# Kernel optimization log

Hardware: AMD Instinct MI355X
Metric: run time of the kernel (lower is better)

Reference implementation:

```python
import jax, jax.numpy as jnp
import numpy as np

B, T, D_IN = 32, 128, 32
H1, H, PEN = 1024, 2048, 1024  # linear1 out, GRU hidden, penultimate
C, P = 64, 4                   # cultivars, phenos


def setup_inputs() -> dict:
    key = jax.random.key(0)
    ks = jax.random.split(key, 22)
    s = 0.02
    inp = {}
    inp['x'] = jax.random.normal(ks[0], (B, T, D_IN), dtype=jnp.float32)
    inp['cultivar_label'] = jax.random.randint(ks[1], (B, 1), 0, C)
    inp['W1'] = jax.random.normal(ks[2], (H1, D_IN), dtype=jnp.float32) * s
    inp['b1'] = jnp.zeros((H1,), jnp.float32)
    inp['W2'] = jax.random.normal(ks[3], (H, H1), dtype=jnp.float32) * s
    inp['b2'] = jnp.zeros((H,), jnp.float32)
    # GRU weights, PyTorch layout: gates stacked (r,z,n) along dim 0
    inp['W_ih'] = jax.random.normal(ks[4], (3 * H, H), dtype=jnp.float32) * s
    inp['b_ih'] = jnp.zeros((3 * H,), jnp.float32)
    inp['W_hh'] = jax.random.normal(ks[5], (3 * H, H), dtype=jnp.float32) * s
    inp['b_hh'] = jnp.zeros((3 * H,), jnp.float32)
    inp['W3'] = jax.random.normal(ks[6], (PEN, H), dtype=jnp.float32) * s
    inp['b3'] = jnp.zeros((PEN,), jnp.float32)
    # per-cultivar expert heads (each a Linear(PEN, 1)) packed as tables
    inp['W4'] = jax.random.normal(ks[7], (C, PEN), dtype=jnp.float32) * s
    inp['b4'] = jnp.zeros((C,), jnp.float32)
    inp['W5'] = jax.random.normal(ks[8], (C, PEN), dtype=jnp.float32) * s
    inp['b5'] = jnp.zeros((C,), jnp.float32)
    inp['W6'] = jax.random.normal(ks[9], (C, PEN), dtype=jnp.float32) * s
    inp['b6'] = jnp.zeros((C,), jnp.float32)
    inp['Wp'] = jax.random.normal(ks[10], (P, C, PEN), dtype=jnp.float32) * s
    inp['bp'] = jnp.zeros((P, C), jnp.float32)
    return inp


def _gru(x_seq, W_ih, b_ih, W_hh, b_hh):
    # x_seq: [B,T,H]; PyTorch GRU gate order (r, z, n)
    Bd, Hd = x_seq.shape[0], W_hh.shape[1]
    xp = jnp.einsum('bth,gh->btg', x_seq, W_ih) + b_ih  # [B,T,3H]

    def step(h, xp_t):
        hp = h @ W_hh.T + b_hh
        xr, xz, xn = jnp.split(xp_t, 3, axis=-1)
        hr, hz, hn = jnp.split(hp, 3, axis=-1)
        r = jax.nn.sigmoid(xr + hr)
        z = jax.nn.sigmoid(xz + hz)
        n = jnp.tanh(xn + r * hn)
        h_new = (1.0 - z) * n + z * h
        return h_new, h_new

    h0 = jnp.zeros((Bd, Hd), x_seq.dtype)
    _, hs = jax.lax.scan(step, h0, jnp.swapaxes(xp, 0, 1))  # [T,B,H]
    return jnp.swapaxes(hs, 0, 1)  # [B,T,H]


def reference(x, cultivar_label, W1, b1, W2, b2, W_ih, b_ih, W_hh, b_hh,
              W3, b3, W4, b4, W5, b5, W6, b6, Wp, bp):
    out = jax.nn.relu(jnp.einsum('btd,hd->bth', x, W1) + b1)
    out = jax.nn.relu(jnp.einsum('bth,gh->btg', out, W2) + b2)
    out = _gru(out, W_ih, b_ih, W_hh, b_hh)
    out_s = jax.nn.relu(jnp.einsum('bth,ph->btp', out, W3) + b3)  # [B,T,PEN]
    labels = cultivar_label[:, 0]

    def head(W, b):  # gather expert row per sample -> [B,T,1]
        return (jnp.einsum('btd,bd->bt', out_s, W[labels]) + b[labels][:, None])[..., None]

    out_lt_10 = head(W4, b4)
    out_lt_50 = head(W5, b5)
    out_lt_90 = head(W6, b6)
    # pheno heads: Wp[:, labels] -> [P,B,PEN]
    out_ph = jax.nn.sigmoid(
        jnp.einsum('btd,pbd->pbt', out_s, Wp[:, labels]) + bp[:, labels][:, :, None]
    )[..., None]  # [P,B,T,1]
    return (out_lt_10, out_lt_50, out_lt_90, out_ph, 0)
```

## Files before the change

kernel.cpp:

```cpp
#include <hip/hip_runtime.h>
#include <hip/hip_bf16.h>
#include <math.h>


typedef __bf16 bf16_t;
typedef __bf16 bf16x4 __attribute__((ext_vector_type(4)));
typedef __bf16 bf16x8 __attribute__((ext_vector_type(8)));
typedef float  f32x4  __attribute__((ext_vector_type(4)));

static __device__ __forceinline__ void zero4(f32x4& v) {
  v[0] = 0.0f; v[1] = 0.0f; v[2] = 0.0f; v[3] = 0.0f;
}

template <typename T>
static __device__ __forceinline__ bf16x8 load8_as_bf16(const T* p);
template <>
__device__ __forceinline__ bf16x8 load8_as_bf16<bf16_t>(const bf16_t* p) {
  return *(const bf16x8*)p;
}
template <>
__device__ __forceinline__ bf16x8 load8_as_bf16<float>(const float* p) {
  bf16x8 v;
#pragma unroll
  for (int u = 0; u < 8; ++u) v[u] = (bf16_t)p[u];
  return v;
}

template <typename TA, typename TB>
__global__ __launch_bounds__(256) void gemm_bt(
    const TA* __restrict__ A, const TB* __restrict__ Bm,
    const float* __restrict__ bias, bf16_t* __restrict__ C,
    int M, int N, int K, int relu)
{
  __shared__ __align__(16) bf16_t As[128 * 32];
  __shared__ __align__(16) bf16_t Bs[128 * 32];

  const int tid  = threadIdx.x;
  const int lane = tid & 63;
  const int wave = tid >> 6;
  const int q    = lane >> 4;
  const int l15  = lane & 15;
  const int wr   = wave >> 1;
  const int wc   = wave & 1;
  const int m0   = blockIdx.y * 128;
  const int n0   = blockIdx.x * 128;

  f32x4 acc[4][4];
#pragma unroll
  for (int i = 0; i < 4; ++i)
#pragma unroll
    for (int j = 0; j < 4; ++j) zero4(acc[i][j]);

  const int se = wave * 512 + lane * 8;

  const int kt_count = K >> 5;
  for (int kt = 0; kt < kt_count; ++kt) {
    const int k0 = kt << 5;

    bf16x8 av[2], bv[2];
#pragma unroll
    for (int c = 0; c < 2; ++c) {
      const int e   = c * 2048 + se;
      const int row = e >> 5;
      const int col = e & 31;
      av[c] = load8_as_bf16<TA>(&A [(size_t)(m0 + row) * K + k0 + col]);
      bv[c] = load8_as_bf16<TB>(&Bm[(size_t)(n0 + row) * K + k0 + col]);
    }

    __syncthreads();
#pragma unroll
    for (int c = 0; c < 2; ++c) {
      *(bf16x8*)&As[c * 2048 + se] = av[c];
      *(bf16x8*)&Bs[c * 2048 + se] = bv[c];
    }
    __syncthreads();

    bf16x8 af[4], bfv[4];
#pragma unroll
    for (int i = 0; i < 4; ++i)
      af[i] = *(const bf16x8*)&As[(wr * 64 + i * 16 + l15) * 32 + q * 8];
#pragma unroll
    for (int j = 0; j < 4; ++j)
      bfv[j] = *(const bf16x8*)&Bs[(wc * 64 + j * 16 + l15) * 32 + q * 8];

#pragma unroll
    for (int i = 0; i < 4; ++i)
#pragma unroll
      for (int j = 0; j < 4; ++j)
        acc[i][j] = __builtin_amdgcn_mfma_f32_16x16x32_bf16(af[i], bfv[j], acc[i][j], 0, 0, 0);
  }

#pragma unroll
  for (int j = 0; j < 4; ++j) {
    const int n = n0 + wc * 64 + j * 16 + l15;
    const float bvl = bias[n];
#pragma unroll
    for (int i = 0; i < 4; ++i) {
      const int mbase = m0 + wr * 64 + i * 16 + q * 4;
#pragma unroll
      for (int r = 0; r < 4; ++r) {
        float v = acc[i][j][r] + bvl;
        if (relu) v = v > 0.0f ? v : 0.0f;
        C[(size_t)(mbase + r) * N + n] = (bf16_t)v;
      }
    }
  }
}

#define WROW 2056

__global__ __launch_bounds__(512, 2) void gru_persistent(
    const float* __restrict__ W_hh, const float* __restrict__ b_hh,
    const bf16_t* __restrict__ xp, bf16_t* __restrict__ hs,
    unsigned* __restrict__ arr)
{
  __shared__ __align__(16) bf16_t Ws[24 * WROW];
  __shared__ __align__(16) float hp_p[8][32][28];

  const int tid  = threadIdx.x;
  const int lane = tid & 63;
  const int wave = tid >> 6;
  const int q    = lane >> 4;
  const int l15  = lane & 15;
  const int j0   = blockIdx.x * 8;
  const int k0w  = wave * 256;

  for (int m = 0; m < 24; ++m) {
    const int gate = m >> 3;
    const float* src = W_hh + (size_t)(gate * 2048 + j0 + (m & 7)) * 2048;
    const int c = tid * 4;
    bf16x4 v;
#pragma unroll
    for (int u = 0; u < 4; ++u) v[u] = (bf16_t)src[c + u];
    *(bf16x4*)&Ws[m * WROW + c] = v;
  }

  const bool pw = tid < 256;
  const int b  = (tid >> 3) & 31;
  const int jj = tid & 7;
  const int jg = j0 + jj;
  float bh_r = 0.f, bh_z = 0.f, bh_n = 0.f;
  if (pw) {
    bh_r = b_hh[jg];
    bh_z = b_hh[2048 + jg];
    bh_n = b_hh[4096 + jg];
  }

  const bf16_t* arow0 = &Ws[(size_t)l15 * WROW + k0w];
  const bf16_t* arow1 = &Ws[(size_t)(16 + (l15 & 7)) * WROW + k0w];

  float hcur = 0.0f;
  unsigned* hs32 = (unsigned*)hs;

  float xr_c = 0.f, xz_c = 0.f, xn_c = 0.f;
  if (pw) {
    xr_c = (float)xp[(size_t)(b * 128 + 0) * 6144 + jg];
    xz_c = (float)xp[(size_t)(b * 128 + 0) * 6144 + 2048 + jg];
    xn_c = (float)xp[(size_t)(b * 128 + 0) * 6144 + 4096 + jg];
  }

  __syncthreads();

  for (int t = 0; t < 128; ++t) {
    if (t > 0) {
      bf16x8 bfr[2][8];
#pragma unroll
      for (int ct = 0; ct < 2; ++ct) {
        const bf16_t* bp_ = hs + ((size_t)(ct * 16 + l15) * 128 + (t - 1)) * 2048
                               + k0w + q * 8;
#pragma unroll
        for (int win = 0; win < 8; ++win)
          bfr[ct][win] = *(const bf16x8*)(bp_ + win * 32);
      }

      f32x4 acc[2][2];
#pragma unroll
      for (int rt = 0; rt < 2; ++rt)
#pragma unroll
        for (int ct = 0; ct < 2; ++ct) zero4(acc[rt][ct]);

#pragma unroll
      for (int win = 0; win < 8; ++win) {
        const bf16x8 a0 = *(const bf16x8*)(arow0 + win * 32 + q * 8);
        const bf16x8 a1 = *(const bf16x8*)(arow1 + win * 32 + q * 8);
        acc[0][0] = __builtin_amdgcn_mfma_f32_16x16x32_bf16(a0, bfr[0][win], acc[0][0], 0, 0, 0);
        acc[0][1] = __builtin_amdgcn_mfma_f32_16x16x32_bf16(a0, bfr[1][win], acc[0][1], 0, 0, 0);
        acc[1][0] = __builtin_amdgcn_mfma_f32_16x16x32_bf16(a1, bfr[0][win], acc[1][0], 0, 0, 0);
        acc[1][1] = __builtin_amdgcn_mfma_f32_16x16x32_bf16(a1, bfr[1][win], acc[1][1], 0, 0, 0);
      }

#pragma unroll
      for (int ct = 0; ct < 2; ++ct) {
        *(f32x4*)&hp_p[wave][ct * 16 + l15][q * 4] = acc[0][ct];
        if (q < 2)
          *(f32x4*)&hp_p[wave][ct * 16 + l15][16 + q * 4] = acc[1][ct];
      }
    }
    __syncthreads();

    if (pw) {
      float pr = 0.0f, pz = 0.0f, pn = 0.0f;
      if (t > 0) {
#pragma unroll
        for (int w = 0; w < 8; ++w) {
          pr += hp_p[w][b][jj];
          pz += hp_p[w][b][8 + jj];
          pn += hp_p[w][b][16 + jj];
        }
      }
      const float r_ = 1.0f / (1.0f + __expf(-(xr_c + pr + bh_r)));
      const float z_ = 1.0f / (1.0f + __expf(-(xz_c + pz + bh_z)));
      const float aa = xn_c + r_ * (pn + bh_n);
      const float et = __expf(-2.0f * aa);
      const float n_ = (1.0f - et) / (1.0f + et);
      hcur = (1.0f - z_) * n_ + z_ * hcur;

      union { bf16_t h; unsigned short u; } cv; cv.h = (bf16_t)hcur;
      const unsigned hv = cv.u;
      const unsigned ov = (unsigned)__shfl_xor((int)hv, 1, 64);
      if ((tid & 1) == 0) {
        const unsigned pk = hv | (ov << 16);
        const size_t widx = ((size_t)b * 128 + t) * 1024 + (jg >> 1);
        __hip_atomic_store(hs32 + widx, pk, __ATOMIC_RELAXED,
                           __HIP_MEMORY_SCOPE_AGENT);
      }
    }

    if (t < 127) {
      asm volatile("s_waitcnt vmcnt(0)" ::: "memory");
      __syncthreads();
      if (tid == 0)
        __hip_atomic_store(arr + (size_t)t * 256 + blockIdx.x, 1u,
                           __ATOMIC_RELAXED, __HIP_MEMORY_SCOPE_AGENT);
      const int tn = t + 1;
      float xr_n = 0.f, xz_n = 0.f, xn_n = 0.f;
      if (pw) {
        xr_n = (float)xp[(size_t)(b * 128 + tn) * 6144 + jg];
        xz_n = (float)xp[(size_t)(b * 128 + tn) * 6144 + 2048 + jg];
        xn_n = (float)xp[(size_t)(b * 128 + tn) * 6144 + 4096 + jg];
      }
      asm volatile("" ::: "memory");

      const unsigned long long* f64p =
          (const unsigned long long*)(arr + (size_t)t * 256) + wave * 16;
      const unsigned long long tgt = 0x0000000100000001ull;
      int guard = 0;
      for (;;) {
        unsigned long long v = tgt;
        if (lane < 16)
          v = __hip_atomic_load(f64p + lane, __ATOMIC_RELAXED,
                                __HIP_MEMORY_SCOPE_AGENT);
        if (__all(v == tgt)) break;
        __builtin_amdgcn_s_sleep(1);
        if (++guard > (1 << 20)) break;
      }

      xr_c = xr_n; xz_c = xz_n; xn_c = xn_n;
    }
  }
}

__global__ __launch_bounds__(256) void heads_kernel(
    const bf16_t* __restrict__ out_s, const int* __restrict__ labels,
    const float* __restrict__ W4, const float* __restrict__ b4,
    const float* __restrict__ W5, const float* __restrict__ b5,
    const float* __restrict__ W6, const float* __restrict__ b6,
    const float* __restrict__ Wp, const float* __restrict__ bp,
    float* __restrict__ out)
{
  const int bt  = blockIdx.x;
  const int b   = bt >> 7;
  const int lab = labels[b];
  const bf16_t* os  = out_s + (size_t)bt * 1024;
  const float* w4  = W4 + (size_t)lab * 1024;
  const float* w5  = W5 + (size_t)lab * 1024;
  const float* w6  = W6 + (size_t)lab * 1024;
  const float* wp0 = Wp + (size_t)lab * 1024;

  float s[7] = {0, 0, 0, 0, 0, 0, 0};
  for (int d = threadIdx.x; d < 1024; d += 256) {
    const float v = (float)os[d];
    s[0] += v * w4[d];
    s[1] += v * w5[d];
    s[2] += v * w6[d];
    s[3] += v * wp0[d];
    s[4] += v * wp0[65536 + d];
    s[5] += v * wp0[131072 + d];
    s[6] += v * wp0[196608 + d];
  }
#pragma unroll
  for (int i = 0; i < 7; ++i)
    for (int off = 32; off > 0; off >>= 1)
      s[i] += __shfl_down(s[i], off, 64);

  __shared__ float red[4][7];
  const int lane = threadIdx.x & 63, wave = threadIdx.x >> 6;
  if (lane == 0)
    for (int i = 0; i < 7; ++i) red[wave][i] = s[i];
  __syncthreads();
  if (threadIdx.x == 0) {
    float tsum[7];
    for (int i = 0; i < 7; ++i)
      tsum[i] = red[0][i] + red[1][i] + red[2][i] + red[3][i];
    out[bt]        = tsum[0] + b4[lab];
    out[4096 + bt] = tsum[1] + b5[lab];
    out[8192 + bt] = tsum[2] + b6[lab];
#pragma unroll
    for (int p = 0; p < 4; ++p) {
      const float v = tsum[3 + p] + bp[p * 64 + lab];
      out[12288 + p * 4096 + bt] = 1.0f / (1.0f + __expf(-v));
    }
  }
}

extern "C" void kernel_launch(void* const* d_in, const int* in_sizes, int n_in,
                              void* d_out, int out_size, void* d_ws, size_t ws_size,
                              hipStream_t stream)
{
  const float* x     = (const float*)d_in[0];
  const int*   label = (const int*)d_in[1];
  const float* W1    = (const float*)d_in[2];
  const float* b1    = (const float*)d_in[3];
  const float* W2    = (const float*)d_in[4];
  const float* b2    = (const float*)d_in[5];
  const float* W_ih  = (const float*)d_in[6];
  const float* b_ih  = (const float*)d_in[7];
  const float* W_hh  = (const float*)d_in[8];
  const float* b_hh  = (const float*)d_in[9];
  const float* W3    = (const float*)d_in[10];
  const float* b3    = (const float*)d_in[11];
  const float* W4    = (const float*)d_in[12];
  const float* b4    = (const float*)d_in[13];
  const float* W5    = (const float*)d_in[14];
  const float* b5    = (const float*)d_in[15];
  const float* W6    = (const float*)d_in[16];
  const float* b6    = (const float*)d_in[17];
  const float* Wp    = (const float*)d_in[18];
  const float* bp    = (const float*)d_in[19];

  char* ws = (char*)d_ws;
  unsigned* arr = (unsigned*)ws;
  bf16_t* out1  = (bf16_t*)(ws + (24u << 20));
  bf16_t* out2  = (bf16_t*)(ws + (32u << 20));
  bf16_t* xp    = (bf16_t*)(ws + (48u << 20));
  bf16_t* hs    = (bf16_t*)(ws + (24u << 20));
  bf16_t* out_s = (bf16_t*)(ws + (40u << 20));
  float*  outp  = (float*)d_out;

  hipMemsetAsync(d_out, 0, (size_t)out_size * sizeof(float), stream);
  hipMemsetAsync(ws, 0, 131072, stream);

  dim3 blk(256);
  gemm_bt<float, float><<<dim3(8, 32), blk, 0, stream>>>(x, W1, b1, out1, 4096, 1024, 32, 1);
  gemm_bt<bf16_t, float><<<dim3(16, 32), blk, 0, stream>>>(out1, W2, b2, out2, 4096, 2048, 1024, 1);
  gemm_bt<bf16_t, float><<<dim3(48, 32), blk, 0, stream>>>(out2, W_ih, b_ih, xp, 4096, 6144, 2048, 0);
  {
    void* gru_args[] = { (void*)&W_hh, (void*)&b_hh, (void*)&xp, (void*)&hs,
                         (void*)&arr };
    hipLaunchCooperativeKernel((void*)gru_persistent, dim3(256), dim3(512),
                               gru_args, 0, stream);
  }
  gemm_bt<bf16_t, float><<<dim3(8, 32), blk, 0, stream>>>(hs, W3, b3, out_s, 4096, 1024, 2048, 1);
  heads_kernel<<<dim3(4096), blk, 0, stream>>>(out_s, label, W4, b4, W5, b5, W6, b6, Wp, bp, outp);
}
```

Before: 1.484 ms.

## Replicate GRU step-arrival flags and stage hidden-state stores via LDS

Each block now publishes its per-step arrival flag into 8 replicated flag arrays, and blocks poll a copy chosen by block index, which is meant to spread contention on the polled cache lines. Hidden-state outputs are gathered in shared memory and written as one 16-byte store per batch row with cache-bypass bits, replacing many 4-byte atomic stores. The wait now happens at the start of the next step, only wave 0 waits for its stores to drain, and the next xp loads move into the gate computation. The flag workspace memset grows to 1 MB to cover the replicated flags. The inline-asm store with sc0 sc1 depends on correct visibility semantics for the cross-block handoff.

```diff
diff --git a/kernel.cpp b/kernel.cpp
--- a/kernel.cpp
+++ b/kernel.cpp
@@ -7,6 +7,7 @@
 typedef __bf16 bf16x4 __attribute__((ext_vector_type(4)));
 typedef __bf16 bf16x8 __attribute__((ext_vector_type(8)));
 typedef float  f32x4  __attribute__((ext_vector_type(4)));
+typedef int    i32x4  __attribute__((ext_vector_type(4)));
 
 static __device__ __forceinline__ void zero4(f32x4& v) {
   v[0] = 0.0f; v[1] = 0.0f; v[2] = 0.0f; v[3] = 0.0f;
@@ -108,6 +109,7 @@
 }
 
 #define WROW 2056
+#define NCOPY 8
 
 __global__ __launch_bounds__(512, 2) void gru_persistent(
     const float* __restrict__ W_hh, const float* __restrict__ b_hh,
@@ -116,13 +118,15 @@
 {
   __shared__ __align__(16) bf16_t Ws[24 * WROW];
   __shared__ __align__(16) float hp_p[8][32][28];
+  __shared__ __align__(16) unsigned short stage[32][8];
 
   const int tid  = threadIdx.x;
   const int lane = tid & 63;
   const int wave = tid >> 6;
   const int q    = lane >> 4;
   const int l15  = lane & 15;
-  const int j0   = blockIdx.x * 8;
+  const int bid  = blockIdx.x;
+  const int j0   = bid * 8;
   const int k0w  = wave * 256;
 
   for (int m = 0; m < 24; ++m) {
@@ -150,7 +154,6 @@
   const bf16_t* arow1 = &Ws[(size_t)(16 + (l15 & 7)) * WROW + k0w];
 
   float hcur = 0.0f;
-  unsigned* hs32 = (unsigned*)hs;
 
   float xr_c = 0.f, xz_c = 0.f, xn_c = 0.f;
   if (pw) {
@@ -163,86 +166,10 @@
 
   for (int t = 0; t < 128; ++t) {
     if (t > 0) {
-      bf16x8 bfr[2][8];
-#pragma unroll
-      for (int ct = 0; ct < 2; ++ct) {
-        const bf16_t* bp_ = hs + ((size_t)(ct * 16 + l15) * 128 + (t - 1)) * 2048
-                               + k0w + q * 8;
-#pragma unroll
-        for (int win = 0; win < 8; ++win)
-          bfr[ct][win] = *(const bf16x8*)(bp_ + win * 32);
-      }
-
-      f32x4 acc[2][2];
-#pragma unroll
-      for (int rt = 0; rt < 2; ++rt)
-#pragma unroll
-        for (int ct = 0; ct < 2; ++ct) zero4(acc[rt][ct]);
-
-#pragma unroll
-      for (int win = 0; win < 8; ++win) {
-        const bf16x8 a0 = *(const bf16x8*)(arow0 + win * 32 + q * 8);
-        const bf16x8 a1 = *(const bf16x8*)(arow1 + win * 32 + q * 8);
-        acc[0][0] = __builtin_amdgcn_mfma_f32_16x16x32_bf16(a0, bfr[0][win], acc[0][0], 0, 0, 0);
-        acc[0][1] = __builtin_amdgcn_mfma_f32_16x16x32_bf16(a0, bfr[1][win], acc[0][1], 0, 0, 0);
-        acc[1][0] = __builtin_amdgcn_mfma_f32_16x16x32_bf16(a1, bfr[0][win], acc[1][0], 0, 0, 0);
-        acc[1][1] = __builtin_amdgcn_mfma_f32_16x16x32_bf16(a1, bfr[1][win], acc[1][1], 0, 0, 0);
-      }
-
-#pragma unroll
-      for (int ct = 0; ct < 2; ++ct) {
-        *(f32x4*)&hp_p[wave][ct * 16 + l15][q * 4] = acc[0][ct];
-        if (q < 2)
-          *(f32x4*)&hp_p[wave][ct * 16 + l15][16 + q * 4] = acc[1][ct];
-      }
-    }
-    __syncthreads();
-
-    if (pw) {
-      float pr = 0.0f, pz = 0.0f, pn = 0.0f;
-      if (t > 0) {
-#pragma unroll
-        for (int w = 0; w < 8; ++w) {
-          pr += hp_p[w][b][jj];
-          pz += hp_p[w][b][8 + jj];
-          pn += hp_p[w][b][16 + jj];
-        }
-      }
-      const float r_ = 1.0f / (1.0f + __expf(-(xr_c + pr + bh_r)));
-      const float z_ = 1.0f / (1.0f + __expf(-(xz_c + pz + bh_z)));
-      const float aa = xn_c + r_ * (pn + bh_n);
-      const float et = __expf(-2.0f * aa);
-      const float n_ = (1.0f - et) / (1.0f + et);
-      hcur = (1.0f - z_) * n_ + z_ * hcur;
-
-      union { bf16_t h; unsigned short u; } cv; cv.h = (bf16_t)hcur;
-      const unsigned hv = cv.u;
-      const unsigned ov = (unsigned)__shfl_xor((int)hv, 1, 64);
-      if ((tid & 1) == 0) {
-        const unsigned pk = hv | (ov << 16);
-        const size_t widx = ((size_t)b * 128 + t) * 1024 + (jg >> 1);
-        __hip_atomic_store(hs32 + widx, pk, __ATOMIC_RELAXED,
-                           __HIP_MEMORY_SCOPE_AGENT);
-      }
-    }
-
-    if (t < 127) {
-      asm volatile("s_waitcnt vmcnt(0)" ::: "memory");
-      __syncthreads();
-      if (tid == 0)
-        __hip_atomic_store(arr + (size_t)t * 256 + blockIdx.x, 1u,
-                           __ATOMIC_RELAXED, __HIP_MEMORY_SCOPE_AGENT);
-      const int tn = t + 1;
-      float xr_n = 0.f, xz_n = 0.f, xn_n = 0.f;
-      if (pw) {
-        xr_n = (float)xp[(size_t)(b * 128 + tn) * 6144 + jg];
-        xz_n = (float)xp[(size_t)(b * 128 + tn) * 6144 + 2048 + jg];
-        xn_n = (float)xp[(size_t)(b * 128 + tn) * 6144 + 4096 + jg];
-      }
-      asm volatile("" ::: "memory");
-
+      const int c = bid & 7;
       const unsigned long long* f64p =
-          (const unsigned long long*)(arr + (size_t)t * 256) + wave * 16;
+          (const unsigned long long*)(arr + ((size_t)(t - 1) * NCOPY + c) * 256)
+          + wave * 16;
       const unsigned long long tgt = 0x0000000100000001ull;
       int guard = 0;
       for (;;) {
@@ -255,6 +182,84 @@
         if (++guard > (1 << 20)) break;
       }
 
+      bf16x8 bfr[2][8];
+#pragma unroll
+      for (int ct = 0; ct < 2; ++ct) {
+        const bf16_t* bp_ = hs + ((size_t)(ct * 16 + l15) * 128 + (t - 1)) * 2048
+                               + k0w + q * 8;
+#pragma unroll
+        for (int win = 0; win < 8; ++win)
+          bfr[ct][win] = *(const bf16x8*)(bp_ + win * 32);
+      }
+
+      f32x4 acc[2][2];
+#pragma unroll
+      for (int rt = 0; rt < 2; ++rt)
+#pragma unroll
+        for (int ct = 0; ct < 2; ++ct) zero4(acc[rt][ct]);
+
+#pragma unroll
+      for (int win = 0; win < 8; ++win) {
+        const bf16x8 a0 = *(const bf16x8*)(arow0 + win * 32 + q * 8);
+        const bf16x8 a1 = *(const bf16x8*)(arow1 + win * 32 + q * 8);
+        acc[0][0] = __builtin_amdgcn_mfma_f32_16x16x32_bf16(a0, bfr[0][win], acc[0][0], 0, 0, 0);
+        acc[0][1] = __builtin_amdgcn_mfma_f32_16x16x32_bf16(a0, bfr[1][win], acc[0][1], 0, 0, 0);
+        acc[1][0] = __builtin_amdgcn_mfma_f32_16x16x32_bf16(a1, bfr[0][win], acc[1][0], 0, 0, 0);
+        acc[1][1] = __builtin_amdgcn_mfma_f32_16x16x32_bf16(a1, bfr[1][win], acc[1][1], 0, 0, 0);
+      }
+
+#pragma unroll
+      for (int ct = 0; ct < 2; ++ct) {
+        *(f32x4*)&hp_p[wave][ct * 16 + l15][q * 4] = acc[0][ct];
+        if (q < 2)
+          *(f32x4*)&hp_p[wave][ct * 16 + l15][16 + q * 4] = acc[1][ct];
+      }
+    }
+    __syncthreads();
+
+    float xr_n = 0.f, xz_n = 0.f, xn_n = 0.f;
+    if (pw) {
+      float pr = 0.0f, pz = 0.0f, pn = 0.0f;
+      if (t > 0) {
+#pragma unroll
+        for (int w = 0; w < 8; ++w) {
+          pr += hp_p[w][b][jj];
+          pz += hp_p[w][b][8 + jj];
+          pn += hp_p[w][b][16 + jj];
+        }
+      }
+      const float r_ = 1.0f / (1.0f + __expf(-(xr_c + pr + bh_r)));
+      const float z_ = 1.0f / (1.0f + __expf(-(xz_c + pz + bh_z)));
+      const float aa = xn_c + r_ * (pn + bh_n);
+      const float et = __expf(-2.0f * aa);
+      const float n_ = (1.0f - et) / (1.0f + et);
+      hcur = (1.0f - z_) * n_ + z_ * hcur;
+
+      if (t < 127) {
+        const int tn = t + 1;
+        xr_n = (float)xp[(size_t)(b * 128 + tn) * 6144 + jg];
+        xz_n = (float)xp[(size_t)(b * 128 + tn) * 6144 + 2048 + jg];
+        xn_n = (float)xp[(size_t)(b * 128 + tn) * 6144 + 4096 + jg];
+      }
+
+      union { bf16_t h; unsigned short u; } cv; cv.h = (bf16_t)hcur;
+      stage[b][jj] = cv.u;
+    }
+    __syncthreads();
+
+    if (wave == 0 && lane < 32) {
+      const i32x4 val = *(const i32x4*)&stage[lane][0];
+      bf16_t* dst = hs + ((size_t)lane * 128 + t) * 2048 + j0;
+      asm volatile("global_store_dwordx4 %0, %1, off sc0 sc1"
+                   :: "v"(dst), "v"(val) : "memory");
+    }
+    if (t < 127) {
+      if (wave == 0) {
+        asm volatile("s_waitcnt vmcnt(0)" ::: "memory");
+        if (lane < NCOPY)
+          __hip_atomic_store(arr + ((size_t)t * NCOPY + lane) * 256 + bid, 1u,
+                             __ATOMIC_RELAXED, __HIP_MEMORY_SCOPE_AGENT);
+      }
       xr_c = xr_n; xz_c = xz_n; xn_c = xn_n;
     }
   }
@@ -348,7 +353,7 @@
   float*  outp  = (float*)d_out;
 
   hipMemsetAsync(d_out, 0, (size_t)out_size * sizeof(float), stream);
-  hipMemsetAsync(ws, 0, 131072, stream);
+  hipMemsetAsync(ws, 0, 1u << 20, stream);
 
   dim3 blk(256);
   gemm_bt<float, float><<<dim3(8, 32), blk, 0, stream>>>(x, W1, b1, out1, 4096, 1024, 32, 1);
```

New measurement: 1.338 ms. -9.8%, faster.
